# Kernel tuning notes

Measured on AMD Instinct MI355X. Metric: run time of the kernel, lower is better.

The kernel has to match this reference:

```python
import jax, jax.numpy as jnp
import numpy as np

VOCAB, EMB, HID = 256, 32, 128
B, T = 512, 512


def setup_inputs() -> dict:
    key = jax.random.key(0)
    ks = jax.random.split(key, 8)
    s_emb = 1.0  # torch nn.Embedding default N(0,1)
    s_lstm = 1.0 / np.sqrt(HID)  # torch LSTM uniform(-1/sqrt(H), 1/sqrt(H))
    s_cls = 1.0 / np.sqrt(HID)
    return {
        "inputs": jax.random.randint(ks[0], (B, T), 0, VOCAB, dtype=jnp.int64),
        "emb": jax.random.normal(ks[1], (VOCAB, EMB), jnp.float32) * s_emb,
        "W_ih": jax.random.uniform(ks[2], (4 * HID, EMB), jnp.float32, -s_lstm, s_lstm),
        "W_hh": jax.random.uniform(ks[3], (4 * HID, HID), jnp.float32, -s_lstm, s_lstm),
        "b_ih": jax.random.uniform(ks[4], (4 * HID,), jnp.float32, -s_lstm, s_lstm),
        "b_hh": jax.random.uniform(ks[5], (4 * HID,), jnp.float32, -s_lstm, s_lstm),
        "W_cls": jax.random.uniform(ks[6], (VOCAB, HID), jnp.float32, -s_cls, s_cls),
        "b_cls": jax.random.uniform(ks[7], (VOCAB,), jnp.float32, -s_cls, s_cls),
    }


def reference(inputs, emb, W_ih, W_hh, b_ih, b_hh, W_cls, b_cls):
    x = emb[inputs]  # [B, T, E]
    H = W_hh.shape[1]
    # Precompute input projections for all timesteps (batched GEMM): [B, T, 4H]
    xw = jnp.einsum("bte,ge->btg", x, W_ih) + b_ih + b_hh
    xw_t = jnp.transpose(xw, (1, 0, 2))  # [T, B, 4H]

    def step(carry, xw_step):
        h, c = carry
        gates = xw_step + h @ W_hh.T  # [B, 4H]
        i, f, g, o = jnp.split(gates, 4, axis=-1)  # torch gate order: i, f, g, o
        i = jax.nn.sigmoid(i)
        f = jax.nn.sigmoid(f)
        g = jnp.tanh(g)
        o = jax.nn.sigmoid(o)
        c = f * c + i * g
        h = o * jnp.tanh(c)
        return (h, c), None

    h0 = jnp.zeros((x.shape[0], H), x.dtype)
    c0 = jnp.zeros((x.shape[0], H), x.dtype)
    (h_last, _), _ = jax.lax.scan(step, (h0, c0), xw_t)
    # classifier on last hidden state: [B, vocab]
    return h_last @ W_cls.T + b_cls
```

## Files before the change

kernel.cpp:

```cpp
#include <hip/hip_runtime.h>
#include <hip/hip_bf16.h>

#define VOCAB 256
#define EMB   32
#define HID   128
#define GATES 512
#define BATCH 512
#define SEQ   512
#define HSTRIDE 144

#define LOG2E 1.442695041f
#if __has_builtin(__builtin_amdgcn_exp2f)
#define GEXP(x) __builtin_amdgcn_exp2f(x)
#define SCALE_IFO LOG2E
#define SCALE_G   (2.0f * LOG2E)
#else
#define GEXP(x) __expf(x)
#define SCALE_IFO 1.0f
#define SCALE_G   2.0f
#endif

#define FAST_BARRIER() asm volatile("s_waitcnt lgkmcnt(0)\n\ts_barrier" ::: "memory")

typedef __attribute__((ext_vector_type(8))) short bf16x8;
typedef __attribute__((ext_vector_type(4))) float f32x4;

static __device__ __forceinline__ unsigned short f2bf(float f) {
  unsigned int u = __float_as_uint(f);
  return (unsigned short)((u + 0x7fffu + ((u >> 16) & 1u)) >> 16);
}

__global__ __launch_bounds__(256) void prep_kernel(
    const float* __restrict__ emb, const float* __restrict__ W_ih,
    const float* __restrict__ b_ih, const float* __restrict__ b_hh,
    float* __restrict__ P) {
  const int wg  = blockIdx.x;
  const int tid = threadIdx.x;
  __shared__ float e[EMB];
  if (tid < EMB) e[tid] = emb[wg * EMB + tid];
  __syncthreads();
  for (int g = tid; g < GATES; g += 256) {
    float acc = b_ih[g] + b_hh[g];
    const float* w = W_ih + g * EMB;
    #pragma unroll
    for (int k = 0; k < EMB; ++k) acc += e[k] * w[k];
    const float sc = ((g >> 7) == 2) ? SCALE_G : SCALE_IFO;
    P[wg * GATES + g] = acc * sc;
  }
}

__global__ __launch_bounds__(512, 2) void lstm_kernel(
    const int* __restrict__ inputs, const float* __restrict__ P,
    const float* __restrict__ W_hh,
    const float* __restrict__ W_cls, const float* __restrict__ b_cls,
    float* __restrict__ out) {
  const int wg   = blockIdx.x;
  const int tid  = threadIdx.x;
  const int wave = tid >> 6;
  const int lane = tid & 63;
  const int c16  = lane & 15;
  const int kg   = lane >> 4;
  const int b0   = wg * 4;

  const int row   = kg;
  const int jfull = wave * 16 + c16;

  __shared__ unsigned int   offs[SEQ][4];
  __shared__ unsigned short hbufA[4 * HSTRIDE];
  __shared__ unsigned short hbufB[4 * HSTRIDE];
  __shared__ float          h_last[4][HID];

  for (int k = tid; k < 4 * SEQ; k += 512) {
    const int r = k & 3, t = k >> 2;
    offs[t][r] = ((unsigned int)(inputs[(b0 + r) * SEQ + t] & 0xff)) << 11;
  }
  for (int k = tid; k < 4 * HSTRIDE; k += 512) { hbufA[k] = 0; hbufB[k] = 0; }

  bf16x8 Bfrag[4][4];
  #pragma unroll
  for (int gt = 0; gt < 4; ++gt) {
    const float sc = (gt == 2) ? SCALE_G : SCALE_IFO;
    const float* wr = W_hh + (gt * 128 + wave * 16 + c16) * HID + kg * 8;
    #pragma unroll
    for (int ks = 0; ks < 4; ++ks) {
      const float4 w0 = *(const float4*)(wr + ks * 32);
      const float4 w1 = *(const float4*)(wr + ks * 32 + 4);
      bf16x8 b;
      b[0] = (short)f2bf(w0.x * sc); b[1] = (short)f2bf(w0.y * sc);
      b[2] = (short)f2bf(w0.z * sc); b[3] = (short)f2bf(w0.w * sc);
      b[4] = (short)f2bf(w1.x * sc); b[5] = (short)f2bf(w1.y * sc);
      b[6] = (short)f2bf(w1.z * sc); b[7] = (short)f2bf(w1.w * sc);
      Bfrag[gt][ks] = b;
    }
  }

  const int aoff = (c16 >> 2) * HSTRIDE + kg * 8;
  const char* PjB = (const char*)(P + jfull);
  float cstate = 0.f;
  float hv = 0.f;

  __syncthreads();

  float p0, p1, p2, p3, q0, q1, q2, q3;
  {
    const float* Pr0 = (const float*)(PjB + offs[0][row]);
    p0 = Pr0[0]; p1 = Pr0[128]; p2 = Pr0[256]; p3 = Pr0[384];
  }

#define STEP(HIN, HOUT, T, PA0, PA1, PA2, PA3, PB0, PB1, PB2, PB3)             \
  {                                                                            \
                          \
    const unsigned short* hb = (HIN) + aoff;                                   \
    const bf16x8 A0 = *(const bf16x8*)(hb);                                    \
    const bf16x8 A1 = *(const bf16x8*)(hb + 32);                               \
    const bf16x8 A2 = *(const bf16x8*)(hb + 64);                               \
    const bf16x8 A3 = *(const bf16x8*)(hb + 96);                               \
          \
    {                                                                          \
      const float* Pn =                                                        \
          (const float*)(PjB + offs[((T) + 1) & (SEQ - 1)][row]);              \
      PB0 = Pn[0]; PB1 = Pn[128]; PB2 = Pn[256]; PB3 = Pn[384];                \
    }                                                                          \
    f32x4 a0 = {}, a1 = {}, a2 = {}, a3 = {};                                  \
    a0 = __builtin_amdgcn_mfma_f32_16x16x32_bf16(A0, Bfrag[0][0], a0, 0,0,0);  \
    a1 = __builtin_amdgcn_mfma_f32_16x16x32_bf16(A0, Bfrag[1][0], a1, 0,0,0);  \
    a2 = __builtin_amdgcn_mfma_f32_16x16x32_bf16(A0, Bfrag[2][0], a2, 0,0,0);  \
    a3 = __builtin_amdgcn_mfma_f32_16x16x32_bf16(A0, Bfrag[3][0], a3, 0,0,0);  \
    a0 = __builtin_amdgcn_mfma_f32_16x16x32_bf16(A1, Bfrag[0][1], a0, 0,0,0);  \
    a1 = __builtin_amdgcn_mfma_f32_16x16x32_bf16(A1, Bfrag[1][1], a1, 0,0,0);  \
    a2 = __builtin_amdgcn_mfma_f32_16x16x32_bf16(A1, Bfrag[2][1], a2, 0,0,0);  \
    a3 = __builtin_amdgcn_mfma_f32_16x16x32_bf16(A1, Bfrag[3][1], a3, 0,0,0);  \
    a0 = __builtin_amdgcn_mfma_f32_16x16x32_bf16(A2, Bfrag[0][2], a0, 0,0,0);  \
    a1 = __builtin_amdgcn_mfma_f32_16x16x32_bf16(A2, Bfrag[1][2], a1, 0,0,0);  \
    a2 = __builtin_amdgcn_mfma_f32_16x16x32_bf16(A2, Bfrag[2][2], a2, 0,0,0);  \
    a3 = __builtin_amdgcn_mfma_f32_16x16x32_bf16(A2, Bfrag[3][2], a3, 0,0,0);  \
    a0 = __builtin_amdgcn_mfma_f32_16x16x32_bf16(A3, Bfrag[0][3], a0, 0,0,0);  \
    a1 = __builtin_amdgcn_mfma_f32_16x16x32_bf16(A3, Bfrag[1][3], a1, 0,0,0);  \
    a2 = __builtin_amdgcn_mfma_f32_16x16x32_bf16(A3, Bfrag[2][3], a2, 0,0,0);  \
    a3 = __builtin_amdgcn_mfma_f32_16x16x32_bf16(A3, Bfrag[3][3], a3, 0,0,0);  \
                   \
    const float iv = __builtin_amdgcn_rcpf(1.f + GEXP(-(a0[0] + PA0)));        \
    const float fv = __builtin_amdgcn_rcpf(1.f + GEXP(-(a1[0] + PA1)));        \
    const float gv = 1.f - 2.f * __builtin_amdgcn_rcpf(GEXP(a2[0] + PA2) + 1.f); \
    const float ov = __builtin_amdgcn_rcpf(1.f + GEXP(-(a3[0] + PA3)));        \
    cstate = fv * cstate + iv * gv;                                            \
    const float th =                                                           \
        1.f - 2.f * __builtin_amdgcn_rcpf(GEXP(cstate * SCALE_G) + 1.f);       \
    hv = ov * th;                                                              \
    unsigned int hpk;                                                          \
    asm("v_cvt_pk_bf16_f32 %0, %1, %2" : "=v"(hpk) : "v"(hv), "v"(hv));        \
    (HOUT)[row * HSTRIDE + jfull] = (unsigned short)hpk;                       \
    FAST_BARRIER();                                                            \
  }

  #pragma unroll 1
  for (int t = 0; t < SEQ; t += 2) {
    STEP(hbufA, hbufB, t,     p0, p1, p2, p3, q0, q1, q2, q3)
    STEP(hbufB, hbufA, t + 1, q0, q1, q2, q3, p0, p1, p2, p3)
  }
#undef STEP

  h_last[row][jfull] = hv;
  __syncthreads();

  const int erow = tid >> 7;
  const int ej   = tid & 127;
  #pragma unroll
  for (int half = 0; half < 2; ++half) {
    const int v = ej + half * 128;
    float acc = b_cls[v];
    const float4* w  = (const float4*)(W_cls + v * HID);
    const float4* hh = (const float4*)&h_last[erow][0];
    #pragma unroll
    for (int k = 0; k < HID / 4; ++k) {
      const float4 wv = w[k];
      const float4 hv4 = hh[k];
      acc += wv.x * hv4.x + wv.y * hv4.y + wv.z * hv4.z + wv.w * hv4.w;
    }
    out[(b0 + erow) * VOCAB + v] = acc;
  }
}

extern "C" void kernel_launch(void* const* d_in, const int* in_sizes, int n_in,
                              void* d_out, int out_size, void* d_ws, size_t ws_size,
                              hipStream_t stream) {
  const int*   inputs = (const int*)d_in[0];
  const float* emb    = (const float*)d_in[1];
  const float* W_ih   = (const float*)d_in[2];
  const float* W_hh   = (const float*)d_in[3];
  const float* b_ih   = (const float*)d_in[4];
  const float* b_hh   = (const float*)d_in[5];
  const float* W_cls  = (const float*)d_in[6];
  const float* b_cls  = (const float*)d_in[7];
  float* outp = (float*)d_out;

  float* Ptab = (float*)d_ws;

  prep_kernel<<<VOCAB, 256, 0, stream>>>(emb, W_ih, b_ih, b_hh, Ptab);
  lstm_kernel<<<BATCH / 4, 512, 0, stream>>>(inputs, Ptab, W_hh, W_cls, b_cls, outp);
}
```

Before: 309.8 us.

## Split LSTM batch across twice as many smaller workgroups of two rows

Each LSTM workgroup now handles 2 batch rows with 4 waves instead of 4 rows with 8 waves, so the grid doubles to 256 blocks and can occupy every CU. Each wave now holds 32 hidden columns of W_hh in registers and issues 32 MFMAs per timestep instead of 16. It selects the relevant accumulator half per lane. This spreads the recurrence across more CUs, but it lengthens each step's serial MFMA chain, wastes more of each 16-row MFMA tile, and raises register pressure, all of which could increase per-step latency.

```diff
diff --git a/kernel.cpp b/kernel.cpp
--- a/kernel.cpp
+++ b/kernel.cpp
@@ -49,7 +49,7 @@
   }
 }
 
-__global__ __launch_bounds__(512, 2) void lstm_kernel(
+__global__ __launch_bounds__(256, 1) void lstm_kernel(
     const int* __restrict__ inputs, const float* __restrict__ P,
     const float* __restrict__ W_hh,
     const float* __restrict__ W_cls, const float* __restrict__ b_cls,
@@ -60,27 +60,30 @@
   const int lane = tid & 63;
   const int c16  = lane & 15;
   const int kg   = lane >> 4;
-  const int b0   = wg * 4;
-
-  const int row   = kg;
-  const int jfull = wave * 16 + c16;
-
-  __shared__ unsigned int   offs[SEQ][4];
-  __shared__ unsigned short hbufA[4 * HSTRIDE];
-  __shared__ unsigned short hbufB[4 * HSTRIDE];
-  __shared__ float          h_last[4][HID];
-
-  for (int k = tid; k < 4 * SEQ; k += 512) {
-    const int r = k & 3, t = k >> 2;
+  const int b0   = wg * 2;
+
+  const int row   = kg >> 1;
+  const int jh    = kg & 1;
+  const int jfull = wave * 32 + jh * 16 + c16;
+
+  __shared__ unsigned int   offs[SEQ][2];
+  __shared__ unsigned short hbufA[2 * HSTRIDE];
+  __shared__ unsigned short hbufB[2 * HSTRIDE];
+  __shared__ float          h_last[2][HID];
+
+  for (int k = tid; k < 2 * SEQ; k += 256) {
+    const int r = k & 1, t = k >> 1;
     offs[t][r] = ((unsigned int)(inputs[(b0 + r) * SEQ + t] & 0xff)) << 11;
   }
-  for (int k = tid; k < 4 * HSTRIDE; k += 512) { hbufA[k] = 0; hbufB[k] = 0; }
-
-  bf16x8 Bfrag[4][4];
+  for (int k = tid; k < 2 * HSTRIDE; k += 256) { hbufA[k] = 0; hbufB[k] = 0; }
+
+  bf16x8 Bfrag[8][4];
   #pragma unroll
-  for (int gt = 0; gt < 4; ++gt) {
+  for (int u = 0; u < 8; ++u) {
+    const int gt = u >> 1;
     const float sc = (gt == 2) ? SCALE_G : SCALE_IFO;
-    const float* wr = W_hh + (gt * 128 + wave * 16 + c16) * HID + kg * 8;
+    const float* wr =
+        W_hh + (gt * 128 + wave * 32 + (u & 1) * 16 + c16) * HID + kg * 8;
     #pragma unroll
     for (int ks = 0; ks < 4; ++ks) {
       const float4 w0 = *(const float4*)(wr + ks * 32);
@@ -90,12 +93,13 @@
       b[2] = (short)f2bf(w0.z * sc); b[3] = (short)f2bf(w0.w * sc);
       b[4] = (short)f2bf(w1.x * sc); b[5] = (short)f2bf(w1.y * sc);
       b[6] = (short)f2bf(w1.z * sc); b[7] = (short)f2bf(w1.w * sc);
-      Bfrag[gt][ks] = b;
+      Bfrag[u][ks] = b;
     }
   }
 
-  const int aoff = (c16 >> 2) * HSTRIDE + kg * 8;
+  const int aoff = (c16 >> 3) * HSTRIDE + kg * 8;
   const char* PjB = (const char*)(P + jfull);
+  const f32x4 ZERO = {};
   float cstate = 0.f;
   float hv = 0.f;
 
@@ -106,6 +110,16 @@
     const float* Pr0 = (const float*)(PjB + offs[0][row]);
     p0 = Pr0[0]; p1 = Pr0[128]; p2 = Pr0[256]; p3 = Pr0[384];
   }
+
+#define MFMA8(AK, KS, CIN0, CIN1, CIN2, CIN3, CIN4, CIN5, CIN6, CIN7)          \
+    a0 = __builtin_amdgcn_mfma_f32_16x16x32_bf16(AK, Bfrag[0][KS], CIN0, 0,0,0); \
+    a1 = __builtin_amdgcn_mfma_f32_16x16x32_bf16(AK, Bfrag[1][KS], CIN1, 0,0,0); \
+    a2 = __builtin_amdgcn_mfma_f32_16x16x32_bf16(AK, Bfrag[2][KS], CIN2, 0,0,0); \
+    a3 = __builtin_amdgcn_mfma_f32_16x16x32_bf16(AK, Bfrag[3][KS], CIN3, 0,0,0); \
+    a4 = __builtin_amdgcn_mfma_f32_16x16x32_bf16(AK, Bfrag[4][KS], CIN4, 0,0,0); \
+    a5 = __builtin_amdgcn_mfma_f32_16x16x32_bf16(AK, Bfrag[5][KS], CIN5, 0,0,0); \
+    a6 = __builtin_amdgcn_mfma_f32_16x16x32_bf16(AK, Bfrag[6][KS], CIN6, 0,0,0); \
+    a7 = __builtin_amdgcn_mfma_f32_16x16x32_bf16(AK, Bfrag[7][KS], CIN7, 0,0,0);
 
 #define STEP(HIN, HOUT, T, PA0, PA1, PA2, PA3, PB0, PB1, PB2, PB3)             \
   {                                                                            \
@@ -121,28 +135,20 @@
           (const float*)(PjB + offs[((T) + 1) & (SEQ - 1)][row]);              \
       PB0 = Pn[0]; PB1 = Pn[128]; PB2 = Pn[256]; PB3 = Pn[384];                \
     }                                                                          \
-    f32x4 a0 = {}, a1 = {}, a2 = {}, a3 = {};                                  \
-    a0 = __builtin_amdgcn_mfma_f32_16x16x32_bf16(A0, Bfrag[0][0], a0, 0,0,0);  \
-    a1 = __builtin_amdgcn_mfma_f32_16x16x32_bf16(A0, Bfrag[1][0], a1, 0,0,0);  \
-    a2 = __builtin_amdgcn_mfma_f32_16x16x32_bf16(A0, Bfrag[2][0], a2, 0,0,0);  \
-    a3 = __builtin_amdgcn_mfma_f32_16x16x32_bf16(A0, Bfrag[3][0], a3, 0,0,0);  \
-    a0 = __builtin_amdgcn_mfma_f32_16x16x32_bf16(A1, Bfrag[0][1], a0, 0,0,0);  \
-    a1 = __builtin_amdgcn_mfma_f32_16x16x32_bf16(A1, Bfrag[1][1], a1, 0,0,0);  \
-    a2 = __builtin_amdgcn_mfma_f32_16x16x32_bf16(A1, Bfrag[2][1], a2, 0,0,0);  \
-    a3 = __builtin_amdgcn_mfma_f32_16x16x32_bf16(A1, Bfrag[3][1], a3, 0,0,0);  \
-    a0 = __builtin_amdgcn_mfma_f32_16x16x32_bf16(A2, Bfrag[0][2], a0, 0,0,0);  \
-    a1 = __builtin_amdgcn_mfma_f32_16x16x32_bf16(A2, Bfrag[1][2], a1, 0,0,0);  \
-    a2 = __builtin_amdgcn_mfma_f32_16x16x32_bf16(A2, Bfrag[2][2], a2, 0,0,0);  \
-    a3 = __builtin_amdgcn_mfma_f32_16x16x32_bf16(A2, Bfrag[3][2], a3, 0,0,0);  \
-    a0 = __builtin_amdgcn_mfma_f32_16x16x32_bf16(A3, Bfrag[0][3], a0, 0,0,0);  \
-    a1 = __builtin_amdgcn_mfma_f32_16x16x32_bf16(A3, Bfrag[1][3], a1, 0,0,0);  \
-    a2 = __builtin_amdgcn_mfma_f32_16x16x32_bf16(A3, Bfrag[2][3], a2, 0,0,0);  \
-    a3 = __builtin_amdgcn_mfma_f32_16x16x32_bf16(A3, Bfrag[3][3], a3, 0,0,0);  \
+    f32x4 a0, a1, a2, a3, a4, a5, a6, a7;                                      \
+    MFMA8(A0, 0, ZERO, ZERO, ZERO, ZERO, ZERO, ZERO, ZERO, ZERO)               \
+    MFMA8(A1, 1, a0, a1, a2, a3, a4, a5, a6, a7)                               \
+    MFMA8(A2, 2, a0, a1, a2, a3, a4, a5, a6, a7)                               \
+    MFMA8(A3, 3, a0, a1, a2, a3, a4, a5, a6, a7)                               \
                    \
-    const float iv = __builtin_amdgcn_rcpf(1.f + GEXP(-(a0[0] + PA0)));        \
-    const float fv = __builtin_amdgcn_rcpf(1.f + GEXP(-(a1[0] + PA1)));        \
-    const float gv = 1.f - 2.f * __builtin_amdgcn_rcpf(GEXP(a2[0] + PA2) + 1.f); \
-    const float ov = __builtin_amdgcn_rcpf(1.f + GEXP(-(a3[0] + PA3)));        \
+    const float gi = jh ? a1[0] : a0[0];                                       \
+    const float gf = jh ? a3[0] : a2[0];                                       \
+    const float gg = jh ? a5[0] : a4[0];                                       \
+    const float go = jh ? a7[0] : a6[0];                                       \
+    const float iv = __builtin_amdgcn_rcpf(1.f + GEXP(-(gi + PA0)));           \
+    const float fv = __builtin_amdgcn_rcpf(1.f + GEXP(-(gf + PA1)));           \
+    const float gv = 1.f - 2.f * __builtin_amdgcn_rcpf(GEXP(gg + PA2) + 1.f);  \
+    const float ov = __builtin_amdgcn_rcpf(1.f + GEXP(-(go + PA3)));           \
     cstate = fv * cstate + iv * gv;                                            \
     const float th =                                                           \
         1.f - 2.f * __builtin_amdgcn_rcpf(GEXP(cstate * SCALE_G) + 1.f);       \
@@ -159,6 +165,7 @@
     STEP(hbufB, hbufA, t + 1, q0, q1, q2, q3, p0, p1, p2, p3)
   }
 #undef STEP
+#undef MFMA8
 
   h_last[row][jfull] = hv;
   __syncthreads();
@@ -197,5 +204,5 @@
   float* Ptab = (float*)d_ws;
 
   prep_kernel<<<VOCAB, 256, 0, stream>>>(emb, W_ih, b_ih, b_hh, Ptab);
-  lstm_kernel<<<BATCH / 4, 512, 0, stream>>>(inputs, Ptab, W_hh, W_cls, b_cls, outp);
-}
+  lstm_kernel<<<BATCH / 2, 256, 0, stream>>>(inputs, Ptab, W_hh, W_cls, b_cls, outp);
+}
```

New measurement: 298.4 us. 1.04x faster.
